# Kernel optimization log

Measured on AMD Instinct MI355X. Metric: run time of the kernel, lower is better.

## Reference

```python
import jax, jax.numpy as jnp
import numpy as np

B, T, C, H = 4, 2048, 1024, 16
HD = C // H  # head dim = 64


def setup_inputs() -> dict:
    key = jax.random.key(0)
    k1, k2, k3 = jax.random.split(key, 3)
    scale_in = 1.0 / np.sqrt(C)
    return {
        "x": jax.random.normal(k1, (B, T, C), dtype=jnp.float32),
        "W_attn": jax.random.normal(k2, (C, 3 * C), dtype=jnp.float32) * scale_in,
        "b_attn": jnp.zeros((3 * C,), dtype=jnp.float32),
        "W_proj": jax.random.normal(k3, (C, C), dtype=jnp.float32) * scale_in,
        "b_proj": jnp.zeros((C,), dtype=jnp.float32),
    }


def reference(x, W_attn, b_attn, W_proj, b_proj):
    b, t, c = x.shape
    qkv = x @ W_attn + b_attn                      # [B,T,3C]
    q, k, v = jnp.split(qkv, 3, axis=-1)
    # [B,T,C] -> [B,H,T,HD]
    def heads(z):
        return z.reshape(b, t, H, HD).transpose(0, 2, 1, 3)
    q, k, v = heads(q), heads(k), heads(v)
    att = jnp.einsum("bhqd,bhkd->bhqk", q, k) / jnp.sqrt(jnp.float32(HD))
    causal = jnp.tril(jnp.ones((t, t), dtype=bool))
    att = jnp.where(causal, att, -jnp.inf)
    att = jax.nn.softmax(att, axis=-1)             # dropout p=0 -> identity
    y = jnp.einsum("bhqk,bhkd->bhqd", att, v)      # [B,H,T,HD]
    y = y.transpose(0, 2, 1, 3).reshape(b, t, c)   # [B,T,C]
    return y @ W_proj + b_proj
```

## Files before the change

### kernel.cpp

```cpp
#include <hip/hip_runtime.h>
#include <hip/hip_bf16.h>

typedef unsigned int u32;
typedef unsigned short u16;
typedef __bf16 bf16x8 __attribute__((ext_vector_type(8)));
typedef float f32x4 __attribute__((ext_vector_type(4)));
typedef _Float16 f16;
typedef _Float16 f16x2 __attribute__((ext_vector_type(2)));
typedef _Float16 f16x4 __attribute__((ext_vector_type(4)));

#define B_ 4
#define T_ 2048
#define C_ 1024
#define H_ 16
#define HD_ 64
#define M_ (B_*T_)
#define N3C (3*C_)
#define N2C (2*C_)

__device__ __forceinline__ u16 f2bf(float f) {
  u32 u = __builtin_bit_cast(u32, f);
  u = (u + 0x7fffu + ((u >> 16) & 1u)) >> 16;
  return (u16)u;
}

#define GLD16(gp, lp) __builtin_amdgcn_global_load_lds( \
    (const __attribute__((address_space(1))) u32*)(gp), \
    (__attribute__((address_space(3))) u32*)(lp), 16, 0, 0)

#if __has_builtin(__builtin_amdgcn_exp2f)
#define EXP2F(x) __builtin_amdgcn_exp2f(x)
#else
#define EXP2F(x) exp2f(x)
#endif

__global__ __launch_bounds__(256) void prep(
    const float* __restrict__ x, const float* __restrict__ Wa,
    const float* __restrict__ Wp,
    u16* __restrict__ xb, u16* __restrict__ W1t, u16* __restrict__ W2t) {
  __shared__ float t[32][33];
  const int blk = blockIdx.x, tid = threadIdx.x;
  if (blk < 8192) {
    int i = blk * 256 + tid;
    float4 v = ((const float4*)x)[i];
    ushort4 o;
    o.x = f2bf(v.x); o.y = f2bf(v.y); o.z = f2bf(v.z); o.w = f2bf(v.w);
    ((ushort4*)xb)[i] = o;
    return;
  }
  const float* W; u16* Wt; int Ndim, id;
  if (blk < 8192 + 3072) { W = Wa; Wt = W1t; Ndim = N3C; id = blk - 8192; }
  else                   { W = Wp; Wt = W2t; Ndim = C_;  id = blk - 11264; }
  const int nt = Ndim / 32;
  const int n0 = (id % nt) * 32, k0 = (id / nt) * 32;
  const int tx = tid & 31, ty = tid >> 5;
  #pragma unroll
  for (int i = ty; i < 32; i += 8)
    t[i][tx] = W[(long)(k0 + i) * Ndim + n0 + tx];
  __syncthreads();
  #pragma unroll
  for (int i = ty; i < 32; i += 8)
    Wt[(long)(n0 + i) * C_ + k0 + tx] = f2bf(t[tx][i]);
}

template<int MODE>
__global__ __launch_bounds__(256) void gemm_bt(
    const u16* __restrict__ A, const u16* __restrict__ Bt,
    const float* __restrict__ bias, void* __restrict__ Cout,
    f16* __restrict__ vt, int N, int K) {
  __shared__ u16 As[128 * 64];
  __shared__ u16 Bs[128 * 64];
  const int tid = threadIdx.x;
  const int wave = tid >> 6, lane = tid & 63;
  const int wm = wave >> 1, wn = wave & 1;
  const int l15 = lane & 15, quad = lane >> 4;
  const int rA = lane >> 3, cxor = (lane & 7) ^ rA;
  const long rowA0 = (long)blockIdx.x * 128;
  const long colB0 = (long)blockIdx.y * 128;

  f32x4 acc[4][4] = {};

  const u16* Ag = A + (rowA0 + wave * 32 + rA) * K + cxor * 8;
  const u16* Bg = Bt + (colB0 + wave * 32 + rA) * K + cxor * 8;
  u16* Asw = &As[(wave * 32) * 64];
  u16* Bsw = &Bs[(wave * 32) * 64];

  for (int k0 = 0; k0 < K; k0 += 64) {
    #pragma unroll
    for (int j = 0; j < 4; ++j) {
      GLD16(Ag + (long)j * 8 * K + k0, Asw + j * 8 * 64);
      GLD16(Bg + (long)j * 8 * K + k0, Bsw + j * 8 * 64);
    }
    __syncthreads();
    #pragma unroll
    for (int kk = 0; kk < 2; ++kk) {
      bf16x8 af[4], bfr[4];
      #pragma unroll
      for (int mt = 0; mt < 4; ++mt) {
        int r = wm * 64 + mt * 16 + l15;
        int c = (kk * 4 + quad) ^ (r & 7);
        af[mt] = *(const bf16x8*)&As[r * 64 + c * 8];
      }
      #pragma unroll
      for (int nt = 0; nt < 4; ++nt) {
        int r = wn * 64 + nt * 16 + l15;
        int c = (kk * 4 + quad) ^ (r & 7);
        bfr[nt] = *(const bf16x8*)&Bs[r * 64 + c * 8];
      }
      #pragma unroll
      for (int mt = 0; mt < 4; ++mt)
        #pragma unroll
        for (int nt = 0; nt < 4; ++nt)
          acc[mt][nt] = __builtin_amdgcn_mfma_f32_16x16x32_bf16(
              af[mt], bfr[nt], acc[mt][nt], 0, 0, 0);
    }
    __syncthreads();
  }

  float bl[4];
  #pragma unroll
  for (int nt = 0; nt < 4; ++nt)
    bl[nt] = bias[colB0 + wn * 64 + nt * 16 + l15];

  const bool vmode = (MODE == 1) && (colB0 >= N2C);
  #pragma unroll
  for (int mt = 0; mt < 4; ++mt) {
    long row = rowA0 + wm * 64 + mt * 16 + quad * 4;
    #pragma unroll
    for (int nt = 0; nt < 4; ++nt) {
      long col = colB0 + wn * 64 + nt * 16 + l15;
      float v0 = acc[mt][nt][0] + bl[nt];
      float v1 = acc[mt][nt][1] + bl[nt];
      float v2 = acc[mt][nt][2] + bl[nt];
      float v3 = acc[mt][nt][3] + bl[nt];
      if (MODE == 0) {
        float* Cf = (float*)Cout;
        Cf[(row + 0) * N + col] = v0;
        Cf[(row + 1) * N + col] = v1;
        Cf[(row + 2) * N + col] = v2;
        Cf[(row + 3) * N + col] = v3;
      } else if (!vmode) {
        u16* qk = (u16*)Cout;
        qk[(row + 0) * N2C + col] = f2bf(v0);
        qk[(row + 1) * N2C + col] = f2bf(v1);
        qk[(row + 2) * N2C + col] = f2bf(v2);
        qk[(row + 3) * N2C + col] = f2bf(v3);
      } else {
        int cv = (int)(col - N2C);
        int hh = cv >> 6, dd = cv & 63;
        int bb = (int)(row >> 11);
        long t = row & 2047;
        f16x2 lo = __builtin_bit_cast(f16x2, __builtin_amdgcn_cvt_pkrtz(v0, v1));
        f16x2 hi = __builtin_bit_cast(f16x2, __builtin_amdgcn_cvt_pkrtz(v2, v3));
        f16x4 w; w[0] = lo[0]; w[1] = lo[1]; w[2] = hi[0]; w[3] = hi[1];
        *(f16x4*)&vt[(((long)bb * H_ + hh) * HD_ + dd) * T_ + t] = w;
      }
    }
  }
}

__global__ __launch_bounds__(256, 6) void flash_attn(
    const u16* __restrict__ qk, const f16* __restrict__ vt,
    u16* __restrict__ yb) {
  __shared__ u16 Ks[2][64 * 64];
  __shared__ f16 Vts[64 * 72];
  const int l = blockIdx.x;
  const int bh = (l & 7) | ((l >> 7) << 3);
  const int bx = (l >> 3) & 15;
  const int b = bh >> 4, h = bh & 15;
  const int tid = threadIdx.x, wave = tid >> 6, lane = tid & 63;
  const int l15 = lane & 15, quad = lane >> 4;
  const int rA = lane >> 3, cxor = (lane & 7) ^ rA;

  const u16* Qb = qk + (long)b * T_ * N2C + h * HD_;
  const f16* Vb = vt + (long)bh * HD_ * T_;
  const u16* Kb0 = Qb + C_ + (long)(wave * 16 + rA) * N2C + cxor * 8;

  const int rv = tid >> 3;
  const int c16 = tid & 7;

  const float cs = 0.125f * 1.44269504088896340736f;

  #pragma unroll 1
  for (int pass = 0; pass < 2; ++pass) {
    const int qt = pass ? bx : 31 - bx;
    const int nKT = qt + 1;
    const int qrow = qt * 64 + wave * 16 + l15;
    const bf16x8 bq0 = *(const bf16x8*)&Qb[(long)qrow * N2C + quad * 8];
    const bf16x8 bq1 = *(const bf16x8*)&Qb[(long)qrow * N2C + 32 + quad * 8];

    float qq = 0.f;
    #pragma unroll
    for (int j = 0; j < 8; ++j) {
      float a = (float)bq0[j], bv = (float)bq1[j];
      qq = __builtin_fmaf(a, a, qq);
      qq = __builtin_fmaf(bv, bv, qq);
    }
    qq += __shfl_xor(qq, 16);
    qq += __shfl_xor(qq, 32);
    const float nref = -qq * cs;

    const u16* kp = Kb0;
    const f16* vp = Vb + (long)rv * T_ + c16 * 8;

    __syncthreads();
    GLD16(kp, &Ks[0][(wave * 16) * 64]);
    GLD16(kp + 8 * N2C, &Ks[0][(wave * 16 + 8) * 64]);
    kp += 64 * N2C;
    uint4 vn0 = *(const uint4*)vp;
    uint4 vn1 = *(const uint4*)(vp + 32 * T_);
    vp += 64;

    float li = 0.f;
    f32x4 o[4] = {};

    for (int kt = 0; kt < nKT; ++kt) {
      const int buf = kt & 1;
      __syncthreads();
      *(uint4*)&Vts[rv * 72 + c16 * 8] = vn0;
      *(uint4*)&Vts[(rv + 32) * 72 + c16 * 8] = vn1;
      __syncthreads();

      if (kt + 1 < nKT) {
        GLD16(kp, &Ks[buf ^ 1][(wave * 16) * 64]);
        GLD16(kp + 8 * N2C, &Ks[buf ^ 1][(wave * 16 + 8) * 64]);
        kp += 64 * N2C;
        vn0 = *(const uint4*)vp;
        vn1 = *(const uint4*)(vp + 32 * T_);
        vp += 64;
      }

      f32x4 St[4] = {};
      #pragma unroll
      for (int kk = 0; kk < 2; ++kk) {
        bf16x8 qf = kk ? bq1 : bq0;
        #pragma unroll
        for (int mt = 0; mt < 4; ++mt) {
          int r = mt * 16 + l15;
          int c = (kk * 4 + quad) ^ (l15 & 7);
          bf16x8 kf = *(const bf16x8*)&Ks[buf][r * 64 + c * 8];
          St[mt] = __builtin_amdgcn_mfma_f32_16x16x32_bf16(kf, qf, St[mt], 0, 0, 0);
        }
      }

      if (kt == qt) {
        #pragma unroll
        for (int mt = 0; mt < 4; ++mt)
          #pragma unroll
          for (int r = 0; r < 4; ++r)
            if (mt * 16 + quad * 4 + r > wave * 16 + l15)
              St[mt][r] = -__builtin_inff();
      }

      float ps = 0.f;
      f16x4 pf[4];
      #pragma unroll
      for (int mt = 0; mt < 4; ++mt) {
        float p0 = EXP2F(__builtin_fmaf(St[mt][0], cs, nref));
        float p1 = EXP2F(__builtin_fmaf(St[mt][1], cs, nref));
        float p2 = EXP2F(__builtin_fmaf(St[mt][2], cs, nref));
        float p3 = EXP2F(__builtin_fmaf(St[mt][3], cs, nref));
        ps += (p0 + p1) + (p2 + p3);
        f16x2 lo = __builtin_bit_cast(f16x2, __builtin_amdgcn_cvt_pkrtz(p0, p1));
        f16x2 hi = __builtin_bit_cast(f16x2, __builtin_amdgcn_cvt_pkrtz(p2, p3));
        pf[mt][0] = lo[0]; pf[mt][1] = lo[1]; pf[mt][2] = hi[0]; pf[mt][3] = hi[1];
      }
      li += ps;

      #pragma unroll
      for (int dt = 0; dt < 4; ++dt) {
        #pragma unroll
        for (int kc = 0; kc < 4; ++kc) {
          f16x4 vf = *(const f16x4*)&Vts[(dt * 16 + l15) * 72 + kc * 16 + quad * 4];
          o[dt] = __builtin_amdgcn_mfma_f32_16x16x16f16(vf, pf[kc], o[dt], 0, 0, 0);
        }
      }
    }

    li += __shfl_xor(li, 16);
    li += __shfl_xor(li, 32);
    float inv = 1.f / li;
    #pragma unroll
    for (int dt = 0; dt < 4; ++dt) {
      ushort4 w;
      w.x = f2bf(o[dt][0] * inv);
      w.y = f2bf(o[dt][1] * inv);
      w.z = f2bf(o[dt][2] * inv);
      w.w = f2bf(o[dt][3] * inv);
      *(ushort4*)&yb[((long)b * T_ + qrow) * C_ + h * HD_ + dt * 16 + quad * 4] = w;
    }
  }
}

extern "C" void kernel_launch(void* const* d_in, const int* in_sizes, int n_in,
                              void* d_out, int out_size, void* d_ws, size_t ws_size,
                              hipStream_t stream) {
  const float* x      = (const float*)d_in[0];
  const float* W_attn = (const float*)d_in[1];
  const float* b_attn = (const float*)d_in[2];
  const float* W_proj = (const float*)d_in[3];
  const float* b_proj = (const float*)d_in[4];
  float* out = (float*)d_out;

  char* ws = (char*)d_ws;
  u16* xb   = (u16*)(ws);
  u16* W1t  = (u16*)(ws + 16777216);
  u16* W2t  = (u16*)(ws + 23068672);
  u16* qkb  = (u16*)(ws + 25165824);
  f16* vtb  = (f16*)(ws + 58720256);
  u16* yb   = (u16*)(ws + 75497472);

  prep<<<dim3(12288), dim3(256), 0, stream>>>(x, W_attn, W_proj, xb, W1t, W2t);
  gemm_bt<1><<<dim3(M_ / 128, N3C / 128), dim3(256), 0, stream>>>(
      xb, W1t, b_attn, qkb, vtb, N3C, C_);
  flash_attn<<<dim3(1024), dim3(256), 0, stream>>>(qkb, vtb, yb);
  gemm_bt<0><<<dim3(M_ / 128, C_ / 128), dim3(256), 0, stream>>>(
      yb, W2t, b_proj, out, nullptr, C_, C_);
}
```

Before: 254.8 us.

## Double-buffer V tile via direct global-to-LDS loads with XOR swizzle

V^T tiles now go straight from global memory into a double-buffered, XOR-swizzled LDS array using the same GLD16 path as K. This replaces the register staging and removes one of the two __syncthreads per key tile. The read pattern for the PV MFMA operands is rewritten to match the swizzle. LDS use grows by one tile and the occupancy hint drops from 6 to 5 blocks per SM.

```diff
diff --git a/kernel.cpp b/kernel.cpp
--- a/kernel.cpp
+++ b/kernel.cpp
@@ -140,11 +140,11 @@
         Cf[(row + 2) * N + col] = v2;
         Cf[(row + 3) * N + col] = v3;
       } else if (!vmode) {
-        u16* qk = (u16*)Cout;
-        qk[(row + 0) * N2C + col] = f2bf(v0);
-        qk[(row + 1) * N2C + col] = f2bf(v1);
-        qk[(row + 2) * N2C + col] = f2bf(v2);
-        qk[(row + 3) * N2C + col] = f2bf(v3);
+        u16* qkp = (u16*)Cout;
+        qkp[(row + 0) * N2C + col] = f2bf(v0);
+        qkp[(row + 1) * N2C + col] = f2bf(v1);
+        qkp[(row + 2) * N2C + col] = f2bf(v2);
+        qkp[(row + 3) * N2C + col] = f2bf(v3);
       } else {
         int cv = (int)(col - N2C);
         int hh = cv >> 6, dd = cv & 63;
@@ -159,11 +159,11 @@
   }
 }
 
-__global__ __launch_bounds__(256, 6) void flash_attn(
+__global__ __launch_bounds__(256, 5) void flash_attn(
     const u16* __restrict__ qk, const f16* __restrict__ vt,
     u16* __restrict__ yb) {
   __shared__ u16 Ks[2][64 * 64];
-  __shared__ f16 Vts[64 * 72];
+  __shared__ f16 Vs[2][64 * 64];
   const int l = blockIdx.x;
   const int bh = (l & 7) | ((l >> 7) << 3);
   const int bx = (l >> 3) & 15;
@@ -173,11 +173,14 @@
   const int rA = lane >> 3, cxor = (lane & 7) ^ rA;
 
   const u16* Qb = qk + (long)b * T_ * N2C + h * HD_;
-  const f16* Vb = vt + (long)bh * HD_ * T_;
+  const f16* Vbase = vt + (long)bh * HD_ * T_;
   const u16* Kb0 = Qb + C_ + (long)(wave * 16 + rA) * N2C + cxor * 8;
-
-  const int rv = tid >> 3;
-  const int c16 = tid & 7;
+  const f16* Vb0 = Vbase + (long)(wave * 16 + rA) * T_ + cxor * 8;
+
+  u16* ksw0 = &Ks[0][(wave * 16) * 64];
+  u16* ksw1 = &Ks[1][(wave * 16) * 64];
+  f16* vsw0 = &Vs[0][(wave * 16) * 64];
+  f16* vsw1 = &Vs[1][(wave * 16) * 64];
 
   const float cs = 0.125f * 1.44269504088896340736f;
 
@@ -201,14 +204,14 @@
     const float nref = -qq * cs;
 
     const u16* kp = Kb0;
-    const f16* vp = Vb + (long)rv * T_ + c16 * 8;
+    const f16* vp = Vb0;
 
     __syncthreads();
-    GLD16(kp, &Ks[0][(wave * 16) * 64]);
-    GLD16(kp + 8 * N2C, &Ks[0][(wave * 16 + 8) * 64]);
+    GLD16(kp, ksw0);
+    GLD16(kp + 8 * N2C, ksw0 + 8 * 64);
+    GLD16(vp, vsw0);
+    GLD16(vp + 8 * T_, vsw0 + 8 * 64);
     kp += 64 * N2C;
-    uint4 vn0 = *(const uint4*)vp;
-    uint4 vn1 = *(const uint4*)(vp + 32 * T_);
     vp += 64;
 
     float li = 0.f;
@@ -217,16 +220,15 @@
     for (int kt = 0; kt < nKT; ++kt) {
       const int buf = kt & 1;
       __syncthreads();
-      *(uint4*)&Vts[rv * 72 + c16 * 8] = vn0;
-      *(uint4*)&Vts[(rv + 32) * 72 + c16 * 8] = vn1;
-      __syncthreads();
 
       if (kt + 1 < nKT) {
-        GLD16(kp, &Ks[buf ^ 1][(wave * 16) * 64]);
-        GLD16(kp + 8 * N2C, &Ks[buf ^ 1][(wave * 16 + 8) * 64]);
+        u16* kd = buf ? ksw0 : ksw1;
+        f16* vd = buf ? vsw0 : vsw1;
+        GLD16(kp, kd);
+        GLD16(kp + 8 * N2C, kd + 8 * 64);
+        GLD16(vp, vd);
+        GLD16(vp + 8 * T_, vd + 8 * 64);
         kp += 64 * N2C;
-        vn0 = *(const uint4*)vp;
-        vn1 = *(const uint4*)(vp + 32 * T_);
         vp += 64;
       }
 
@@ -271,7 +273,9 @@
       for (int dt = 0; dt < 4; ++dt) {
         #pragma unroll
         for (int kc = 0; kc < 4; ++kc) {
-          f16x4 vf = *(const f16x4*)&Vts[(dt * 16 + l15) * 72 + kc * 16 + quad * 4];
+          int slot = (2 * kc + (quad >> 1)) ^ (l15 & 7);
+          f16x4 vf = *(const f16x4*)&Vs[buf][(dt * 16 + l15) * 64 +
+                                            slot * 8 + (quad & 1) * 4];
           o[dt] = __builtin_amdgcn_mfma_f32_16x16x16f16(vf, pf[kc], o[dt], 0, 0, 0);
         }
       }
```

New measurement: 250.1 us. About the same (-1.9%).
